# Optimization experiments

Hardware: AMD Instinct MI355X
Metric: run time of the kernel (lower is better)

Reference implementation:

```python
import jax, jax.numpy as jnp
import numpy as np
import math

B, L, D, H, DFF = 2, 2048, 1024, 16, 4096

def _mha(xq, xkv, Wq, bq, Wk, bk, Wv, bv, Wo, bo, mask, h):
    # xq: [B,Lq,D], xkv: [B,Lk,D], mask: [B,1,Lq,Lk] bool
    b, lq, d = xq.shape
    dk = d // h
    q = (xq @ Wq + bq).reshape(b, lq, h, dk).transpose(0, 2, 1, 3)        # [B,h,Lq,dk]
    k = (xkv @ Wk + bk).reshape(b, -1, h, dk).transpose(0, 2, 1, 3)       # [B,h,Lk,dk]
    v = (xkv @ Wv + bv).reshape(b, -1, h, dk).transpose(0, 2, 1, 3)       # [B,h,Lk,dk]
    scores = jnp.einsum('bhqd,bhkd->bhqk', q, k) / jnp.sqrt(jnp.float32(dk))
    scores = jnp.where(mask, scores, jnp.float32(-1e9))                   # masked_fill(mask==0, -1e9)
    prob = jax.nn.softmax(scores, axis=-1)
    out = jnp.einsum('bhqk,bhkd->bhqd', prob, v)
    out = out.transpose(0, 2, 1, 3).reshape(b, lq, d)
    return out @ Wo + bo

def setup_inputs() -> dict:
    key = jax.random.key(0)
    ks = jax.random.split(key, 16)
    s = 0.02
    inp = {
        'tgt': jax.random.normal(ks[0], (B, L, D), jnp.float32),
        'encoder_out': jax.random.normal(ks[1], (B, L, D), jnp.float32),
        'tgt_mask': jnp.broadcast_to(jnp.tril(jnp.ones((L, L), bool)), (B, 1, L, L)),
        'src_tgt_mask': jnp.ones((B, 1, L, L), bool),
    }
    names = ['sWq','sWk','sWv','sWo','cWq','cWk','cWv','cWo']
    for i, n in enumerate(names):
        inp[n] = s * jax.random.normal(ks[2 + i], (D, D), jnp.float32)
        inp['sb' + n[2] if n[0] == 's' else 'cb' + n[2]] = jnp.zeros((D,), jnp.float32)
    inp['W1'] = s * jax.random.normal(ks[10], (D, DFF), jnp.float32)
    inp['b1'] = jnp.zeros((DFF,), jnp.float32)
    inp['W2'] = s * jax.random.normal(ks[11], (DFF, D), jnp.float32)
    inp['b2'] = jnp.zeros((D,), jnp.float32)
    return inp

def reference(tgt, encoder_out, tgt_mask, src_tgt_mask,
              sWq, sbq, sWk, sbk, sWv, sbv, sWo, sbo,
              cWq, cbq, cWk, cbk, cWv, cbv, cWo, cbo,
              W1, b1, W2, b2):
    # residual 1: masked self-attention (no norm)
    x = tgt + _mha(tgt, tgt, sWq, sbq, sWk, sbk, sWv, sbv, sWo, sbo, tgt_mask, H)
    # residual 2: cross-attention over encoder_out
    x = x + _mha(x, encoder_out, cWq, cbq, cWk, cbk, cWv, cbv, cWo, cbo, src_tgt_mask, H)
    # residual 3: position-wise FFN with ReLU
    x = x + (jax.nn.relu(x @ W1 + b1) @ W2 + b2)
    return x
```

## Files before the change

### kernel.cpp

```cpp
#include <hip/hip_runtime.h>

typedef unsigned short u16;
typedef unsigned int u32;
typedef __attribute__((ext_vector_type(8))) short short8;
typedef __attribute__((ext_vector_type(8))) __bf16 bf16x8;
typedef __attribute__((ext_vector_type(4))) float f32x4;
typedef __attribute__((ext_vector_type(4))) u16 u16x4;
typedef __attribute__((ext_vector_type(2))) u32 u32x2;

#define GLD16(gp, lp) __builtin_amdgcn_global_load_lds( \
    (const __attribute__((address_space(1))) unsigned int*)(gp), \
    (__attribute__((address_space(3))) unsigned int*)(lp), 16, 0, 0)

#define WAITCNT_VM(N) asm volatile("s_waitcnt vmcnt(" #N ")" ::: "memory")

#if defined(__has_builtin) && __has_builtin(__builtin_amdgcn_exp2f)
#define EXP2(x) __builtin_amdgcn_exp2f(x)
#else
static __device__ __forceinline__ float exp2_asm(float x){
  float r; asm("v_exp_f32 %0, %1" : "=v"(r) : "v"(x)); return r;
}
#define EXP2(x) exp2_asm(x)
#endif

__device__ __forceinline__ float bf2f(u16 u){
  unsigned x = ((unsigned)u) << 16; float f; __builtin_memcpy(&f, &x, 4); return f;
}
__device__ __forceinline__ u16 f2bf(float f){
  unsigned x; __builtin_memcpy(&x, &f, 4);
  x += 0x7fffu + ((x >> 16) & 1u);
  return (u16)(x >> 16);
}
__device__ __forceinline__ u32 pkhi(float lo, float hi){
  u32 a, b; __builtin_memcpy(&a, &lo, 4); __builtin_memcpy(&b, &hi, 4);
  return __builtin_amdgcn_perm(b, a, 0x07060302u);
}
__device__ __forceinline__ f32x4 mfma_bf16(short8 a, short8 b, f32x4 c){
  return __builtin_amdgcn_mfma_f32_16x16x32_bf16(
      __builtin_bit_cast(bf16x8, a), __builtin_bit_cast(bf16x8, b), c, 0, 0, 0);
}

__global__ __launch_bounds__(256) void k_conv(const float* __restrict__ s, u16* __restrict__ d, int n){
  int i4 = (blockIdx.x * 256 + threadIdx.x) * 4;
  if (i4 < n){
    float4 v = *(const float4*)(s + i4);
    u16x4 o; o.x = f2bf(v.x); o.y = f2bf(v.y); o.z = f2bf(v.z); o.w = f2bf(v.w);
    *(u16x4*)(d + i4) = o;
  }
}

__global__ __launch_bounds__(256) void k_transpose(const float* __restrict__ s, u16* __restrict__ d, int K, int N){
  __shared__ float t[32][33];
  int bx = blockIdx.x * 32, by = blockIdx.y * 32;
  int x = threadIdx.x & 31, y = threadIdx.x >> 5;
  #pragma unroll
  for (int i = 0; i < 4; i++)
    t[y + i*8][x] = s[(size_t)(by + y + i*8) * N + bx + x];
  __syncthreads();
  #pragma unroll
  for (int i = 0; i < 4; i++)
    d[(size_t)(bx + y + i*8) * K + by + x] = f2bf(t[x][y + i*8]);
}

struct TP8 { const float* s[8]; u16* d[8]; };
__global__ __launch_bounds__(256) void k_transpose8(TP8 p){
  __shared__ float t[32][33];
  const float* s = p.s[blockIdx.z];
  u16* d = p.d[blockIdx.z];
  int bx = blockIdx.x * 32, by = blockIdx.y * 32;
  int x = threadIdx.x & 31, y = threadIdx.x >> 5;
  #pragma unroll
  for (int i = 0; i < 4; i++)
    t[y + i*8][x] = s[(size_t)(by + y + i*8) * 1024 + bx + x];
  __syncthreads();
  #pragma unroll
  for (int i = 0; i < 4; i++)
    d[(size_t)(bx + y + i*8) * 1024 + by + x] = f2bf(t[x][y + i*8]);
}

__global__ __launch_bounds__(256) void k_packbias(
    const float* __restrict__ sbq, const float* __restrict__ sbk,
    const float* __restrict__ sbv, const float* __restrict__ cbk,
    const float* __restrict__ cbv, float* __restrict__ pbS,
    float* __restrict__ pbC){
  int i = blockIdx.x * 256 + threadIdx.x;
  if (i < 3072) pbS[i] = (i < 1024) ? sbq[i] : (i < 2048 ? sbk[i-1024] : sbv[i-2048]);
  if (i < 2048) pbC[i] = (i < 1024) ? cbk[i] : cbv[i-1024];
}

template<int EPI>
__global__ __launch_bounds__(256, 2) void k_gemm_bt(
    const u16* __restrict__ A, const u16* __restrict__ BT,
    const float* __restrict__ bias,
    u16* __restrict__ outB,
    int M, int N, int K, int vt_start, u16* __restrict__ Vt){
  __shared__ u16 As[3][128*32];
  __shared__ u16 Bs[3][128*32];
  int tid = threadIdx.x, wave = tid >> 6, lane = tid & 63;
  int bm = blockIdx.x * 128, bn = blockIdx.y * 128;
  int wm = (wave & 1) * 64, wn = (wave >> 1) * 64;
  int l15 = lane & 15, quad = lane >> 4;

  f32x4 z = {0.f, 0.f, 0.f, 0.f};
  f32x4 acc[4][4];
  #pragma unroll
  for (int a = 0; a < 4; a++)
    #pragma unroll
    for (int b = 0; b < 4; b++) acc[a][b] = z;

  int sr = wave*16 + (lane >> 2);
  int sc = (lane & 3) * 8;
  const u16* Ag = A  + (size_t)(bm + sr) * K + sc;
  const u16* Bg = BT + (size_t)(bn + sr) * K + sc;
  int NK = K >> 5;

  auto stage = [&](int k0, int s){
    GLD16(Ag + k0,                &As[s][(wave*16     ) * 32]);
    GLD16(Ag + (size_t)64*K + k0, &As[s][(wave*16 + 64) * 32]);
    GLD16(Bg + k0,                &Bs[s][(wave*16     ) * 32]);
    GLD16(Bg + (size_t)64*K + k0, &Bs[s][(wave*16 + 64) * 32]);
  };
  stage(0, 0);
  stage(32, 1);

  for (int kt = 0; kt < NK; kt++){
    if (kt + 1 < NK) { WAITCNT_VM(4); } else { WAITCNT_VM(0); }
    __builtin_amdgcn_s_barrier();
    int nt = kt + 2;
    if (nt < NK) stage(nt * 32, nt % 3);
    int cur = kt % 3;
    short8 af[4], bf[4];
    #pragma unroll
    for (int mi = 0; mi < 4; mi++)
      af[mi] = *(const short8*)&As[cur][(wm + mi*16 + l15)*32 + quad*8];
    #pragma unroll
    for (int ni = 0; ni < 4; ni++)
      bf[ni] = *(const short8*)&Bs[cur][(wn + ni*16 + l15)*32 + quad*8];
    #pragma unroll
    for (int mi = 0; mi < 4; mi++)
      #pragma unroll
      for (int ni = 0; ni < 4; ni++)
        acc[mi][ni] = mfma_bf16(af[mi], bf[ni], acc[mi][ni]);
  }

  #pragma unroll
  for (int mi = 0; mi < 4; mi++){
    #pragma unroll
    for (int ni = 0; ni < 4; ni++){
      int col = bn + wn + ni*16 + l15;
      float bv = bias[col];
      if (EPI == 0 && col >= vt_start){
        int vc = col - vt_start;
        int hh = vc >> 6, dd = vc & 63;
        int row0 = bm + wm + mi*16 + quad*4;
        int bb = row0 >> 11, ll = row0 & 2047;
        u16x4 vv;
        #pragma unroll
        for (int r = 0; r < 4; r++) vv[r] = f2bf(acc[mi][ni][r] + bv);
        *(u16x4*)&Vt[(((size_t)bb*16 + hh)*64 + dd)*2048 + ll] = vv;
      } else {
        #pragma unroll
        for (int r = 0; r < 4; r++){
          int row = bm + wm + mi*16 + quad*4 + r;
          float v = acc[mi][ni][r] + bv;
          if (EPI == 1) v = v > 0.f ? v : 0.f;
          outB[(size_t)row * N + col] = f2bf(v);
        }
      }
    }
  }
}

template<int EPI>
__global__ __launch_bounds__(256, 2) void k_gemm_n64(
    const u16* __restrict__ A, const u16* __restrict__ BT,
    const float* __restrict__ bias, const float* __restrict__ resid,
    float* __restrict__ outF, u16* __restrict__ outB,
    int M, int N, int K){
  __shared__ u16 As[3][64*32];
  __shared__ u16 Bs[3][128*32];
  int tid = threadIdx.x, wave = tid >> 6, lane = tid & 63;
  int bm = blockIdx.x * 64, bn = blockIdx.y * 128;
  int wn = wave * 32;
  int l15 = lane & 15, quad = lane >> 4;

  f32x4 z = {0.f, 0.f, 0.f, 0.f};
  f32x4 acc[4][2];
  #pragma unroll
  for (int a = 0; a < 4; a++)
    #pragma unroll
    for (int b = 0; b < 2; b++) acc[a][b] = z;

  int sr = wave*16 + (lane >> 2);
  int sc = (lane & 3) * 8;
  const u16* Ag = A  + (size_t)(bm + sr) * K + sc;
  const u16* Bg = BT + (size_t)(bn + sr) * K + sc;
  int NK = K >> 5;

  auto stage = [&](int k0, int s){
    GLD16(Ag + k0,                &As[s][(wave*16     ) * 32]);
    GLD16(Bg + k0,                &Bs[s][(wave*16     ) * 32]);
    GLD16(Bg + (size_t)64*K + k0, &Bs[s][(wave*16 + 64) * 32]);
  };
  stage(0, 0);
  stage(32, 1);

  for (int kt = 0; kt < NK; kt++){
    if (kt + 1 < NK) { WAITCNT_VM(3); } else { WAITCNT_VM(0); }
    __builtin_amdgcn_s_barrier();
    int nt = kt + 2;
    if (nt < NK) stage(nt * 32, nt % 3);
    int cur = kt % 3;
    short8 af[4], bf[2];
    #pragma unroll
    for (int mi = 0; mi < 4; mi++)
      af[mi] = *(const short8*)&As[cur][(mi*16 + l15)*32 + quad*8];
    #pragma unroll
    for (int ni = 0; ni < 2; ni++)
      bf[ni] = *(const short8*)&Bs[cur][(wn + ni*16 + l15)*32 + quad*8];
    #pragma unroll
    for (int mi = 0; mi < 4; mi++)
      #pragma unroll
      for (int ni = 0; ni < 2; ni++)
        acc[mi][ni] = mfma_bf16(af[mi], bf[ni], acc[mi][ni]);
  }

  #pragma unroll
  for (int mi = 0; mi < 4; mi++){
    #pragma unroll
    for (int ni = 0; ni < 2; ni++){
      int col = bn + wn + ni*16 + l15;
      float bv = bias[col];
      #pragma unroll
      for (int r = 0; r < 4; r++){
        int row = bm + mi*16 + quad*4 + r;
        float v = acc[mi][ni][r] + bv;
        size_t idx = (size_t)row * N + col;
        if (EPI >= 2) v += resid[idx];
        if (EPI == 2 || EPI == 3) outF[idx] = v;
        if (EPI != 3) outB[idx] = f2bf(v);
      }
    }
  }
}

template<bool CAUSAL>
__global__ __launch_bounds__(256, 2) void k_flash(
    const u16* __restrict__ Q, int ldq,
    const u16* __restrict__ Kg, int ldk,
    const u16* __restrict__ Vt,
    u16* __restrict__ O, int ldo){
  __shared__ u16 Ks[128*64];
  __shared__ u16 Vs[64*128];
  __shared__ u16 Ps[128*128];
  int tid = threadIdx.x, wave = tid >> 6, lane = tid & 63;
  int l15 = lane & 15, quad = lane >> 4;
  int bx = blockIdx.x;
  int qt = CAUSAL ? ((bx & 1) ? (15 - (bx >> 1)) : (bx >> 1)) : bx;
  int bh = blockIdx.y;
  int b = bh >> 4, h = bh & 15;
  size_t bL = (size_t)b * 2048;
  const u16* qp = Q  + (bL + qt*128) * (size_t)ldq + h*64;
  const u16* kp = Kg + bL * (size_t)ldk + h*64;
  const u16* vtp = Vt + (size_t)bh * 64 * 2048;
  int wm = wave * 32;

  const float QSCALE = 0.125f * 1.44269504088896f;
  short8 qf[2][2];
  #pragma unroll
  for (int mi = 0; mi < 2; mi++)
    #pragma unroll
    for (int ks = 0; ks < 2; ks++){
      short8 t = *(const short8*)(qp + (size_t)(wm + mi*16 + l15)*ldq + ks*32 + quad*8);
      #pragma unroll
      for (int j = 0; j < 8; j++)
        t[j] = (short)f2bf(bf2f((u16)t[j]) * QSCALE);
      qf[mi][ks] = t;
    }

  f32x4 z = {0.f, 0.f, 0.f, 0.f};
  f32x4 o[2][4];
  float mrow[2], lrow[2];
  #pragma unroll
  for (int mi = 0; mi < 2; mi++){ mrow[mi] = -3.0e38f; lrow[mi] = 0.f; }
  #pragma unroll
  for (int mi = 0; mi < 2; mi++)
    #pragma unroll
    for (int nd = 0; nd < 4; nd++) o[mi][nd] = z;

  int nkt = CAUSAL ? (qt + 1) : 16;
  for (int kt = 0; kt < nkt; kt++){
    int cg = ((lane & 7) ^ ((lane >> 3) & 7)) * 8;
    #pragma unroll
    for (int i = 0; i < 4; i++){
      int r = i*32 + wave*8 + (lane >> 3);
      GLD16(kp + (size_t)(kt*128 + r) * ldk + cg, &Ks[(i*32 + wave*8) * 64]);
    }
    #pragma unroll
    for (int i = 0; i < 4; i++){
      int d0 = i*16 + wave*4;
      int d = d0 + (lane >> 4);
      int j = lane & 15;
      int chunk = (j & 8) | ((j ^ (d & 7)) & 7);
      GLD16(vtp + (size_t)d*2048 + kt*128 + chunk*8, &Vs[d0*128]);
    }
    __syncthreads();

    f32x4 s[2][8];
    #pragma unroll
    for (int mi = 0; mi < 2; mi++)
      #pragma unroll
      for (int nk = 0; nk < 8; nk++) s[mi][nk] = z;
    #pragma unroll
    for (int ks = 0; ks < 2; ks++){
      short8 kf[8];
      #pragma unroll
      for (int nk = 0; nk < 8; nk++){
        int row = nk*16 + l15;
        kf[nk] = *(const short8*)&Ks[row*64 + (((ks*4 + quad) ^ (row & 7)))*8];
      }
      #pragma unroll
      for (int mi = 0; mi < 2; mi++)
        #pragma unroll
        for (int nk = 0; nk < 8; nk++)
          s[mi][nk] = mfma_bf16(kf[nk], qf[mi][ks], s[mi][nk]);
    }

    if (CAUSAL && kt == qt){
      #pragma unroll
      for (int mi = 0; mi < 2; mi++){
        int q = wm + mi*16 + l15;
        #pragma unroll
        for (int nk = 0; nk < 8; nk++)
          #pragma unroll
          for (int r = 0; r < 4; r++){
            int key = nk*16 + quad*4 + r;
            if (key > q) s[mi][nk][r] = -1e30f;
          }
      }
    }

    #pragma unroll
    for (int mi = 0; mi < 2; mi++){
      float mx = s[mi][0][0];
      #pragma unroll
      for (int nk = 0; nk < 8; nk++)
        #pragma unroll
        for (int r = 0; r < 4; r++) mx = fmaxf(mx, s[mi][nk][r]);
      mx = fmaxf(mx, __shfl_xor(mx, 16));
      mx = fmaxf(mx, __shfl_xor(mx, 32));
      float mnew = fmaxf(mrow[mi], mx);
      float alpha = EXP2(mrow[mi] - mnew);
      mrow[mi] = mnew;
      float ls = 0.f;
      #pragma unroll
      for (int nk = 0; nk < 8; nk++)
        #pragma unroll
        for (int r = 0; r < 4; r++){
          float p = EXP2(s[mi][nk][r] - mnew);
          s[mi][nk][r] = p;
          ls += p;
        }
      ls += __shfl_xor(ls, 16);
      ls += __shfl_xor(ls, 32);
      lrow[mi] = lrow[mi] * alpha + ls;
      #pragma unroll
      for (int r = 0; r < 4; r++){
        float ar = __shfl(alpha, quad*20 + r);
        #pragma unroll
        for (int nd = 0; nd < 4; nd++) o[mi][nd][r] *= ar;
      }
    }

    #pragma unroll
    for (int mi = 0; mi < 2; mi++){
      int row = wm + mi*16 + l15;
      #pragma unroll
      for (int nk = 0; nk < 8; nk++){
        u32x2 pw;
        pw.x = pkhi(s[mi][nk][0], s[mi][nk][1]);
        pw.y = pkhi(s[mi][nk][2], s[mi][nk][3]);
        int c = nk*4 + quad;
        int phys = c ^ (row & 14);
        *(u32x2*)&Ps[row*128 + phys*4] = pw;
      }
    }

    #pragma unroll
    for (int kc = 0; kc < 4; kc++){
      short8 vf[4], pf[2];
      #pragma unroll
      for (int nd = 0; nd < 4; nd++){
        int d = nd*16 + l15;
        int cc = kc*4 + quad;
        int phys = (cc & 8) | ((cc ^ (d & 7)) & 7);
        vf[nd] = *(const short8*)&Vs[d*128 + phys*8];
      }
      #pragma unroll
      for (int mi = 0; mi < 2; mi++){
        int row = wm + mi*16 + l15;
        int c = kc*8 + quad*2;
        int phys = c ^ (row & 14);
        pf[mi] = *(const short8*)&Ps[row*128 + phys*4];
      }
      #pragma unroll
      for (int mi = 0; mi < 2; mi++)
        #pragma unroll
        for (int nd = 0; nd < 4; nd++)
          o[mi][nd] = mfma_bf16(pf[mi], vf[nd], o[mi][nd]);
    }
    __syncthreads();
  }

  u16* op = O + (bL + qt*128) * (size_t)ldo + h*64;
  #pragma unroll
  for (int mi = 0; mi < 2; mi++){
    float invl = 1.f / lrow[mi];
    #pragma unroll
    for (int r = 0; r < 4; r++){
      float ir = __shfl(invl, quad*20 + r);
      #pragma unroll
      for (int nd = 0; nd < 4; nd++)
        op[(size_t)(wm + mi*16 + quad*4 + r)*ldo + nd*16 + l15] = f2bf(o[mi][nd][r] * ir);
    }
  }
}

extern "C" void kernel_launch(void* const* d_in, const int* in_sizes, int n_in,
                              void* d_out, int out_size, void* d_ws, size_t ws_size,
                              hipStream_t stream){
  (void)in_sizes; (void)n_in; (void)out_size; (void)ws_size;
  const float* tgt = (const float*)d_in[0];
  const float* enc = (const float*)d_in[1];
  const float* sWq = (const float*)d_in[4];  const float* sbq = (const float*)d_in[5];
  const float* sWk = (const float*)d_in[6];  const float* sbk = (const float*)d_in[7];
  const float* sWv = (const float*)d_in[8];  const float* sbv = (const float*)d_in[9];
  const float* sWo = (const float*)d_in[10]; const float* sbo = (const float*)d_in[11];
  const float* cWq = (const float*)d_in[12]; const float* cbq = (const float*)d_in[13];
  const float* cWk = (const float*)d_in[14]; const float* cbk = (const float*)d_in[15];
  const float* cWv = (const float*)d_in[16]; const float* cbv = (const float*)d_in[17];
  const float* cWo = (const float*)d_in[18]; const float* cbo = (const float*)d_in[19];
  const float* W1  = (const float*)d_in[20]; const float* b1  = (const float*)d_in[21];
  const float* W2  = (const float*)d_in[22]; const float* b2  = (const float*)d_in[23];
  float* out = (float*)d_out;

  const int M = 4096;
  const int NEVER = 1 << 30;
  char* w = (char*)d_ws;
  auto alloc = [&](size_t bytes)->void*{ void* p = w; w += (bytes + 255) & ~(size_t)255; return p; };
  u16* tb    = (u16*)alloc((size_t)M*1024*2);
  u16* eb    = (u16*)alloc((size_t)M*1024*2);
  u16* qkv   = (u16*)alloc((size_t)M*3072*2);
  u16* ao    = (u16*)alloc((size_t)M*1024*2);
  u16* xb    = (u16*)alloc((size_t)M*1024*2);
  float* x1f = (float*)alloc((size_t)M*1024*4);
  u16* hbuf  = (u16*)alloc((size_t)M*4096*2);
  u16* VtS   = (u16*)alloc((size_t)32*64*2048*2);
  u16* VtC   = (u16*)alloc((size_t)32*64*2048*2);
  u16* sQKVT = (u16*)alloc((size_t)3072*1024*2);
  u16* sWoT  = (u16*)alloc((size_t)1024*1024*2);
  u16* cWqT  = (u16*)alloc((size_t)1024*1024*2);
  u16* cKVT  = (u16*)alloc((size_t)2048*1024*2);
  u16* cWoT  = (u16*)alloc((size_t)1024*1024*2);
  u16* W1T   = (u16*)alloc((size_t)4096*1024*2);
  u16* W2T   = (u16*)alloc((size_t)1024*4096*2);
  float* pbS = (float*)alloc(3072*4);
  float* pbC = (float*)alloc(2048*4);
  u16* cq  = tb;
  u16* ckv = qkv;

  k_conv<<<dim3(4096), 256, 0, stream>>>(tgt, tb, M*1024);
  k_conv<<<dim3(4096), 256, 0, stream>>>(enc, eb, M*1024);
  TP8 tp;
  tp.s[0]=sWq; tp.s[1]=sWk; tp.s[2]=sWv; tp.s[3]=sWo;
  tp.s[4]=cWq; tp.s[5]=cWk; tp.s[6]=cWv; tp.s[7]=cWo;
  tp.d[0]=sQKVT; tp.d[1]=sQKVT+1024*1024; tp.d[2]=sQKVT+2048*1024; tp.d[3]=sWoT;
  tp.d[4]=cWqT; tp.d[5]=cKVT; tp.d[6]=cKVT+1024*1024; tp.d[7]=cWoT;
  k_transpose8<<<dim3(32,32,8), 256, 0, stream>>>(tp);
  k_transpose<<<dim3(128,32), 256, 0, stream>>>(W1, W1T, 1024, 4096);
  k_transpose<<<dim3(32,128), 256, 0, stream>>>(W2, W2T, 4096, 1024);
  k_packbias<<<dim3(12), 256, 0, stream>>>(sbq, sbk, sbv, cbk, cbv, pbS, pbC);

  k_gemm_bt<0><<<dim3(32,24), 256, 0, stream>>>(tb, sQKVT, pbS, qkv, M, 3072, 1024, 2048, VtS);
  k_flash<true><<<dim3(16,32), 256, 0, stream>>>(qkv, 3072, qkv+1024, 3072, VtS, ao, 1024);
  k_gemm_n64<2><<<dim3(64,8), 256, 0, stream>>>(ao, sWoT, sbo, tgt, x1f, xb, M, 1024, 1024);

  k_gemm_n64<0><<<dim3(64,8), 256, 0, stream>>>(xb, cWqT, cbq, nullptr, nullptr, cq, M, 1024, 1024);
  k_gemm_bt<0><<<dim3(32,16), 256, 0, stream>>>(eb, cKVT, pbC, ckv, M, 2048, 1024, 1024, VtC);
  k_flash<false><<<dim3(16,32), 256, 0, stream>>>(cq, 1024, ckv, 2048, VtC, ao, 1024);
  k_gemm_n64<2><<<dim3(64,8), 256, 0, stream>>>(ao, cWoT, cbo, x1f, x1f, xb, M, 1024, 1024);

  k_gemm_bt<1><<<dim3(32,32), 256, 0, stream>>>(xb, W1T, b1, hbuf, M, 4096, 1024, NEVER, nullptr);
  k_gemm_n64<3><<<dim3(64,8), 256, 0, stream>>>(hbuf, W2T, b2, x1f, out, nullptr, M, 1024, 4096);
}
```

Baseline: 579.3 us.

## Deepen GEMM pipelines to four stages and split-K the FFN down-projection

Both GEMM kernels move from a 3-stage to a 4-stage global-to-LDS ring with three tiles in flight, and the vmcnt waits are adjusted to match. The n64 kernel's launch bound is raised to 3 blocks per SM. The W2 GEMM (K=4096) is split across two z-slices that atomically add into a zeroed fp32 output, with bias and residual added only by slice 0. This aims to hide more load latency and to double the blocks for the long-K GEMM, at the cost of more LDS per block, an extra memset and atomic traffic, and a non-deterministic summation order.

```diff
diff --git a/kernel.cpp b/kernel.cpp
--- a/kernel.cpp
+++ b/kernel.cpp
@@ -94,8 +94,8 @@
     const float* __restrict__ bias,
     u16* __restrict__ outB,
     int M, int N, int K, int vt_start, u16* __restrict__ Vt){
-  __shared__ u16 As[3][128*32];
-  __shared__ u16 Bs[3][128*32];
+  __shared__ u16 As[4][128*32];
+  __shared__ u16 Bs[4][128*32];
   int tid = threadIdx.x, wave = tid >> 6, lane = tid & 63;
   int bm = blockIdx.x * 128, bn = blockIdx.y * 128;
   int wm = (wave & 1) * 64, wn = (wave >> 1) * 64;
@@ -122,13 +122,16 @@
   };
   stage(0, 0);
   stage(32, 1);
+  stage(64, 2);
 
   for (int kt = 0; kt < NK; kt++){
-    if (kt + 1 < NK) { WAITCNT_VM(4); } else { WAITCNT_VM(0); }
+    if (kt < NK-2)      { WAITCNT_VM(8); }
+    else if (kt == NK-2){ WAITCNT_VM(4); }
+    else                { WAITCNT_VM(0); }
     __builtin_amdgcn_s_barrier();
-    int nt = kt + 2;
-    if (nt < NK) stage(nt * 32, nt % 3);
-    int cur = kt % 3;
+    int nt = kt + 3;
+    if (nt < NK) stage(nt * 32, nt & 3);
+    int cur = kt & 3;
     short8 af[4], bf[4];
     #pragma unroll
     for (int mi = 0; mi < 4; mi++)
@@ -172,17 +175,18 @@
 }
 
 template<int EPI>
-__global__ __launch_bounds__(256, 2) void k_gemm_n64(
+__global__ __launch_bounds__(256, 3) void k_gemm_n64(
     const u16* __restrict__ A, const u16* __restrict__ BT,
     const float* __restrict__ bias, const float* __restrict__ resid,
     float* __restrict__ outF, u16* __restrict__ outB,
-    int M, int N, int K){
-  __shared__ u16 As[3][64*32];
-  __shared__ u16 Bs[3][128*32];
+    int M, int N, int K, int lda){
+  __shared__ u16 As[4][64*32];
+  __shared__ u16 Bs[4][128*32];
   int tid = threadIdx.x, wave = tid >> 6, lane = tid & 63;
   int bm = blockIdx.x * 64, bn = blockIdx.y * 128;
   int wn = wave * 32;
   int l15 = lane & 15, quad = lane >> 4;
+  int koff = (EPI == 4) ? blockIdx.z * K : 0;
 
   f32x4 z = {0.f, 0.f, 0.f, 0.f};
   f32x4 acc[4][2];
@@ -193,24 +197,27 @@
 
   int sr = wave*16 + (lane >> 2);
   int sc = (lane & 3) * 8;
-  const u16* Ag = A  + (size_t)(bm + sr) * K + sc;
-  const u16* Bg = BT + (size_t)(bn + sr) * K + sc;
+  const u16* Ag = A  + (size_t)(bm + sr) * lda + sc + koff;
+  const u16* Bg = BT + (size_t)(bn + sr) * lda + sc + koff;
   int NK = K >> 5;
 
   auto stage = [&](int k0, int s){
-    GLD16(Ag + k0,                &As[s][(wave*16     ) * 32]);
-    GLD16(Bg + k0,                &Bs[s][(wave*16     ) * 32]);
-    GLD16(Bg + (size_t)64*K + k0, &Bs[s][(wave*16 + 64) * 32]);
+    GLD16(Ag + k0,                  &As[s][(wave*16     ) * 32]);
+    GLD16(Bg + k0,                  &Bs[s][(wave*16     ) * 32]);
+    GLD16(Bg + (size_t)64*lda + k0, &Bs[s][(wave*16 + 64) * 32]);
   };
   stage(0, 0);
   stage(32, 1);
+  stage(64, 2);
 
   for (int kt = 0; kt < NK; kt++){
-    if (kt + 1 < NK) { WAITCNT_VM(3); } else { WAITCNT_VM(0); }
+    if (kt < NK-2)      { WAITCNT_VM(6); }
+    else if (kt == NK-2){ WAITCNT_VM(3); }
+    else                { WAITCNT_VM(0); }
     __builtin_amdgcn_s_barrier();
-    int nt = kt + 2;
-    if (nt < NK) stage(nt * 32, nt % 3);
-    int cur = kt % 3;
+    int nt = kt + 3;
+    if (nt < NK) stage(nt * 32, nt & 3);
+    int cur = kt & 3;
     short8 af[4], bf[2];
     #pragma unroll
     for (int mi = 0; mi < 4; mi++)
@@ -234,11 +241,17 @@
       #pragma unroll
       for (int r = 0; r < 4; r++){
         int row = bm + mi*16 + quad*4 + r;
-        float v = acc[mi][ni][r] + bv;
+        float v = acc[mi][ni][r];
         size_t idx = (size_t)row * N + col;
-        if (EPI >= 2) v += resid[idx];
-        if (EPI == 2 || EPI == 3) outF[idx] = v;
-        if (EPI != 3) outB[idx] = f2bf(v);
+        if (EPI == 4){
+          if (blockIdx.z == 0) v += bv + resid[idx];
+          unsafeAtomicAdd(&outF[idx], v);
+        } else {
+          v += bv;
+          if (EPI >= 2) v += resid[idx];
+          if (EPI == 2 || EPI == 3) outF[idx] = v;
+          if (EPI != 3) outB[idx] = f2bf(v);
+        }
       }
     }
   }
@@ -483,13 +496,14 @@
 
   k_gemm_bt<0><<<dim3(32,24), 256, 0, stream>>>(tb, sQKVT, pbS, qkv, M, 3072, 1024, 2048, VtS);
   k_flash<true><<<dim3(16,32), 256, 0, stream>>>(qkv, 3072, qkv+1024, 3072, VtS, ao, 1024);
-  k_gemm_n64<2><<<dim3(64,8), 256, 0, stream>>>(ao, sWoT, sbo, tgt, x1f, xb, M, 1024, 1024);
-
-  k_gemm_n64<0><<<dim3(64,8), 256, 0, stream>>>(xb, cWqT, cbq, nullptr, nullptr, cq, M, 1024, 1024);
+  k_gemm_n64<2><<<dim3(64,8), 256, 0, stream>>>(ao, sWoT, sbo, tgt, x1f, xb, M, 1024, 1024, 1024);
+
+  k_gemm_n64<0><<<dim3(64,8), 256, 0, stream>>>(xb, cWqT, cbq, nullptr, nullptr, cq, M, 1024, 1024, 1024);
   k_gemm_bt<0><<<dim3(32,16), 256, 0, stream>>>(eb, cKVT, pbC, ckv, M, 2048, 1024, 1024, VtC);
   k_flash<false><<<dim3(16,32), 256, 0, stream>>>(cq, 1024, ckv, 2048, VtC, ao, 1024);
-  k_gemm_n64<2><<<dim3(64,8), 256, 0, stream>>>(ao, cWoT, cbo, x1f, x1f, xb, M, 1024, 1024);
+  k_gemm_n64<2><<<dim3(64,8), 256, 0, stream>>>(ao, cWoT, cbo, x1f, x1f, xb, M, 1024, 1024, 1024);
 
   k_gemm_bt<1><<<dim3(32,32), 256, 0, stream>>>(xb, W1T, b1, hbuf, M, 4096, 1024, NEVER, nullptr);
-  k_gemm_n64<3><<<dim3(64,8), 256, 0, stream>>>(hbuf, W2T, b2, x1f, out, nullptr, M, 1024, 4096);
-}
+  hipMemsetAsync(out, 0, (size_t)M*1024*4, stream);
+  k_gemm_n64<4><<<dim3(64,8,2), 256, 0, stream>>>(hbuf, W2T, b2, x1f, out, nullptr, M, 1024, 2048, 4096);
+}
```

Measured after the change: 605.7 us. 1.05x slower.
